# Optimization experiments

Hardware: AMD Instinct MI355X
Metric: run time of the kernel (lower is better)

## Reference

```python
import jax, jax.numpy as jnp
import numpy as np

N_DRUG, N_TARGET, N_EDGES, H = 50000, 20000, 500000, 256


def setup_inputs() -> dict:
    key = jax.random.key(0)
    ks = jax.random.split(key, 6)
    s = 1.0 / np.sqrt(2 * H)
    return {
        "z_drug": jax.random.normal(ks[0], (N_DRUG, H), dtype=jnp.float32),
        "z_target": jax.random.normal(ks[1], (N_TARGET, H), dtype=jnp.float32),
        "row": jax.random.randint(ks[2], (N_EDGES,), 0, N_DRUG, dtype=jnp.int64),
        "col": jax.random.randint(ks[3], (N_EDGES,), 0, N_TARGET, dtype=jnp.int64),
        "W1": jax.random.normal(ks[4], (2 * H, H), dtype=jnp.float32) * s,
        "b1": jnp.zeros((H,), dtype=jnp.float32),
        "W2": jax.random.normal(ks[5], (H, 1), dtype=jnp.float32) * (1.0 / np.sqrt(H)),
        "b2": jnp.zeros((1,), dtype=jnp.float32),
    }


def reference(z_drug, z_target, row, col, W1, b1, W2, b2):
    # gather endpoint embeddings by edge index, concat -> [E, 2H]
    zc = jnp.concatenate([z_drug[row], z_target[col]], axis=-1)
    h = jax.nn.relu(zc @ W1 + b1)          # [E, H]
    return h @ W2 + b2                     # [E, 1]
```

## Files before the change

### kernel.cpp

```cpp
#include <hip/hip_runtime.h>
#include <hip/hip_bf16.h>
#include <stdint.h>


typedef unsigned short u16;
typedef __attribute__((ext_vector_type(8))) short short8;
typedef __attribute__((ext_vector_type(4))) float f32x4;

#define HDIM 256
#define KDIM 512
#define BK 64
#define BIN_SHIFT 4

__device__ __forceinline__ u16 f2bf(float f) {
  union { float f; uint32_t u; } v; v.f = f;
  uint32_t u = v.u;
  return (u16)((u + 0x7fffu + ((u >> 16) & 1u)) >> 16);
}
__device__ __forceinline__ u16 f2h(float f) {
  union { _Float16 h; u16 u; } v; v.h = (_Float16)f;
  return v.u;
}
__device__ __forceinline__ float h2f(u16 b) {
  union { _Float16 h; u16 u; } v; v.u = b;
  return (float)v.h;
}

__device__ __forceinline__ void gl2lds16(const void* g, void* l) {
  __builtin_amdgcn_global_load_lds(
      (const __attribute__((address_space(1))) unsigned int*)g,
      (__attribute__((address_space(3))) unsigned int*)l,
      16, 0, 0);
}

__global__ void prep_w1t(const float* __restrict__ w1, u16* __restrict__ w1t) {
  const int b = blockIdx.x;
  __shared__ float tile[64][65];
  const int k0 = (b >> 2) * 64, n0 = (b & 3) * 64;
  const int tx = threadIdx.x & 63, ty = threadIdx.x >> 6;
#pragma unroll
  for (int i = ty; i < 64; i += 4)
    tile[i][tx] = w1[(size_t)(k0 + i) * HDIM + n0 + tx];
  __syncthreads();
#pragma unroll
  for (int i = ty; i < 64; i += 4)
    w1t[(size_t)(n0 + i) * KDIM + k0 + tx] = f2bf(tile[tx][i]);
}

__global__ void hist_kernel(const int* __restrict__ row, int* __restrict__ bins,
                            int E, int NB) {
  __shared__ int lh[4096];
  for (int i = threadIdx.x; i < NB; i += 256) lh[i] = 0;
  __syncthreads();
  for (int e = blockIdx.x * 256 + threadIdx.x; e < E; e += gridDim.x * 256)
    atomicAdd(&lh[row[e] >> BIN_SHIFT], 1);
  __syncthreads();
  for (int i = threadIdx.x; i < NB; i += 256) {
    int c = lh[i];
    if (c) atomicAdd(&bins[i], c);
  }
}

__global__ void scan_kernel(int* __restrict__ bins, int NB) {
  __shared__ int part[256];
  const int t = threadIdx.x;
  const int per = (NB + 255) / 256;
  const int lo = t * per, hi = min(lo + per, NB);
  int s = 0;
  for (int i = lo; i < hi; ++i) s += bins[i];
  part[t] = s;
  __syncthreads();
  if (t == 0) {
    int a = 0;
    for (int i = 0; i < 256; ++i) { int c = part[i]; part[i] = a; a += c; }
  }
  __syncthreads();
  int run = part[t];
  for (int i = lo; i < hi; ++i) { int c = bins[i]; bins[i] = run; run += c; }
}

__global__ void scatter_kernel(const int* __restrict__ row,
                               int* __restrict__ cursor,
                               int* __restrict__ perm, int E) {
  for (int e = blockIdx.x * 256 + threadIdx.x; e < E; e += gridDim.x * 256) {
    int pos = atomicAdd(&cursor[row[e] >> BIN_SHIFT], 1);
    perm[pos] = e;
  }
}

__global__ __launch_bounds__(256, 2) void uv_gemm(
    const float* __restrict__ zdf, const float* __restrict__ ztf,
    const u16* __restrict__ w1t, const float* __restrict__ b1,
    u16* __restrict__ Uh, u16* __restrict__ Vh,
    int ND, int NT, int nUb) {
  __shared__ u16 lB[2][HDIM * BK];

  const int bid = blockIdx.x;
  const int isV = (bid >= nUb);
  const int lb  = isV ? (bid - nUb) : bid;
  const float* zf = isV ? ztf : zdf;
  u16* Oh = isV ? Vh : Uh;
  const int NR = isV ? NT : ND;
  const int r0 = lb * 128;
  const int kb = isV ? 4 : 0;

  const int tid   = threadIdx.x;
  const int wid   = tid >> 6;
  const int lane  = tid & 63;
  const int r8    = lane >> 3;
  const int slog  = ((lane & 7) ^ (r8 & 7)) * 8;
  const int colid = lane & 15;
  const int quad  = lane >> 4;
  const int csw   = colid & 7;

  const u16* pB = w1t + (uint32_t)(wid * 64 + r8) * KDIM + slog;
  u16* lBw0 = &lB[0][(wid * 64) * BK];
  u16* lBw1 = &lB[1][(wid * 64) * BK];

  uint32_t offR[2];
#pragma unroll
  for (int rt = 0; rt < 2; ++rt) {
    int r = min(r0 + wid * 32 + rt * 16 + colid, NR - 1);
    offR[rt] = (uint32_t)r * HDIM;
  }

  f32x4 acc[2][16];
#pragma unroll
  for (int i = 0; i < 2; ++i)
#pragma unroll
    for (int j = 0; j < 16; ++j) acc[i][j] = f32x4{0.f, 0.f, 0.f, 0.f};

  float4 a32[2][2][2];
  short8 aB[2][2][2];

  auto loadA = [&](int kc) {
#pragma unroll
    for (int rt = 0; rt < 2; ++rt)
#pragma unroll
      for (int s = 0; s < 2; ++s) {
        const float* p = zf + offR[rt] + kc * BK + s * 32 + quad * 8;
        a32[rt][s][0] = ((const float4*)p)[0];
        a32[rt][s][1] = ((const float4*)p)[1];
      }
  };
  auto cvtA = [&](int buf) {
#pragma unroll
    for (int rt = 0; rt < 2; ++rt)
#pragma unroll
      for (int s = 0; s < 2; ++s) {
        float4 lo = a32[rt][s][0], hi = a32[rt][s][1];
        short8 r;
        r[0] = (short)f2bf(lo.x); r[1] = (short)f2bf(lo.y);
        r[2] = (short)f2bf(lo.z); r[3] = (short)f2bf(lo.w);
        r[4] = (short)f2bf(hi.x); r[5] = (short)f2bf(hi.y);
        r[6] = (short)f2bf(hi.z); r[7] = (short)f2bf(hi.w);
        aB[buf][rt][s] = r;
      }
  };
  auto stageB = [&](int kch, u16* dst) {
#pragma unroll
    for (int t = 0; t < 8; ++t)
      gl2lds16(pB + (size_t)t * 8 * KDIM + kch * BK, dst + t * 8 * BK);
  };

  loadA(0);
  stageB(kb, lBw0);
  asm volatile("s_waitcnt vmcnt(0)" ::: "memory");
  cvtA(0);
  __builtin_amdgcn_s_barrier();

#pragma unroll
  for (int kc = 0; kc < 4; ++kc) {
    const int cur = kc & 1, nxt = cur ^ 1;
    if (kc < 3) {
      loadA(kc + 1);
      stageB(kb + kc + 1, nxt ? lBw1 : lBw0);
    }
#pragma unroll
    for (int s = 0; s < 2; ++s) {
      const int sl = s * 4 + quad;
      __builtin_amdgcn_s_setprio(1);
#pragma unroll
      for (int ct = 0; ct < 16; ++ct) {
        short8 bF = *(const short8*)
            &lB[cur][(ct * 16 + colid) * BK + ((sl ^ csw) * 8)];
        acc[0][ct] = __builtin_amdgcn_mfma_f32_16x16x32_bf16(
            aB[cur][0][s], bF, acc[0][ct], 0, 0, 0);
        acc[1][ct] = __builtin_amdgcn_mfma_f32_16x16x32_bf16(
            aB[cur][1][s], bF, acc[1][ct], 0, 0, 0);
      }
      __builtin_amdgcn_s_setprio(0);
    }
    if (kc < 3) {
      asm volatile("s_waitcnt vmcnt(0)" ::: "memory");
      cvtA(nxt);
      __builtin_amdgcn_s_barrier();
    }
  }

  float b1v[16];
#pragma unroll
  for (int ct = 0; ct < 16; ++ct)
    b1v[ct] = isV ? 0.f : b1[ct * 16 + colid];
#pragma unroll
  for (int rt = 0; rt < 2; ++rt)
#pragma unroll
    for (int j = 0; j < 4; ++j) {
      int r = r0 + wid * 32 + rt * 16 + quad * 4 + j;
      if (r < NR) {
#pragma unroll
        for (int ct = 0; ct < 16; ++ct)
          Oh[(size_t)r * HDIM + ct * 16 + colid] =
              f2h(acc[rt][ct][j] + b1v[ct]);
      }
    }
}

__global__ __launch_bounds__(256, 8) void edge_kernel_sorted(
    const u16* __restrict__ U, const u16* __restrict__ V,
    const int* __restrict__ perm,
    const int* __restrict__ row, const int* __restrict__ col,
    const float* __restrict__ w2, const float* __restrict__ b2,
    float* __restrict__ out, int E) {
  const int tid  = threadIdx.x;
  const int lane = tid & 63;
  const int wid  = tid >> 6;
  const int li   = lane & 7;
  const int eg   = lane >> 3;

  float w2v[32];
#pragma unroll
  for (int i = 0; i < 32; ++i) w2v[i] = w2[li * 32 + i];
  const float b2v = b2[0];

  for (int base = blockIdx.x * 32; base < E; base += gridDim.x * 32) {
    const int idx = base + wid * 8 + eg;
    const int ii  = min(idx, E - 1);
    const int pe  = perm[ii];
    const short8* up = (const short8*)(U + (size_t)row[pe] * HDIM + li * 32);
    const short8* vp = (const short8*)(V + (size_t)col[pe] * HDIM + li * 32);
    short8 ub[4], vb[4];
#pragma unroll
    for (int t = 0; t < 4; ++t) { ub[t] = up[t]; vb[t] = vp[t]; }
    float s = 0.f;
#pragma unroll
    for (int t = 0; t < 4; ++t)
#pragma unroll
      for (int i = 0; i < 8; ++i) {
        float h = h2f((u16)ub[t][i]) + h2f((u16)vb[t][i]);
        s += fmaxf(h, 0.f) * w2v[t * 8 + i];
      }
    s += __shfl_xor(s, 1, 8);
    s += __shfl_xor(s, 2, 8);
    s += __shfl_xor(s, 4, 8);
    if (li == 0 && idx < E) out[pe] = s + b2v;
  }
}

__global__ __launch_bounds__(256, 8) void edge_kernel(
    const u16* __restrict__ U, const u16* __restrict__ V,
    const int* __restrict__ row, const int* __restrict__ col,
    const float* __restrict__ w2, const float* __restrict__ b2,
    float* __restrict__ out, int E) {
  const int tid  = threadIdx.x;
  const int lane = tid & 63;
  const int wid  = tid >> 6;
  const int li   = lane & 7;
  const int eg   = lane >> 3;
  float w2v[32];
#pragma unroll
  for (int i = 0; i < 32; ++i) w2v[i] = w2[li * 32 + i];
  const float b2v = b2[0];
  for (int base = blockIdx.x * 32; base < E; base += gridDim.x * 32) {
    const int e  = base + wid * 8 + eg;
    const int ee = min(e, E - 1);
    const short8* up = (const short8*)(U + (size_t)row[ee] * HDIM + li * 32);
    const short8* vp = (const short8*)(V + (size_t)col[ee] * HDIM + li * 32);
    short8 ub[4], vb[4];
#pragma unroll
    for (int t = 0; t < 4; ++t) { ub[t] = up[t]; vb[t] = vp[t]; }
    float s = 0.f;
#pragma unroll
    for (int t = 0; t < 4; ++t)
#pragma unroll
      for (int i = 0; i < 8; ++i) {
        float h = h2f((u16)ub[t][i]) + h2f((u16)vb[t][i]);
        s += fmaxf(h, 0.f) * w2v[t * 8 + i];
      }
    s += __shfl_xor(s, 1, 8);
    s += __shfl_xor(s, 2, 8);
    s += __shfl_xor(s, 4, 8);
    if (li == 0 && e < E) out[e] = s + b2v;
  }
}

__global__ void fallback_kernel(
    const float* __restrict__ zd, const float* __restrict__ zt,
    const int* __restrict__ row, const int* __restrict__ col,
    const float* __restrict__ W1, const float* __restrict__ b1,
    const float* __restrict__ W2, const float* __restrict__ b2,
    float* __restrict__ out, int E) {
  __shared__ float zc[16][512];
  __shared__ float red[4][16];
  const int e0 = blockIdx.x * 16;
  const int tid = threadIdx.x;
  for (int i = tid; i < 16 * 512; i += 256) {
    int e = i >> 9, k = i & 511;
    int ge = min(e0 + e, E - 1);
    zc[e][k] = (k < HDIM) ? zd[(size_t)row[ge] * HDIM + k]
                          : zt[(size_t)col[ge] * HDIM + (k - HDIM)];
  }
  __syncthreads();
  float acc[16];
#pragma unroll
  for (int e = 0; e < 16; ++e) acc[e] = 0.f;
  for (int k = 0; k < KDIM; ++k) {
    float w = W1[k * HDIM + tid];
#pragma unroll
    for (int e = 0; e < 16; ++e) acc[e] += zc[e][k] * w;
  }
  float wv = W2[tid], bv = b1[tid];
  const int lane = tid & 63, wid = tid >> 6;
#pragma unroll
  for (int e = 0; e < 16; ++e) {
    float pv = fmaxf(acc[e] + bv, 0.f) * wv;
#pragma unroll
    for (int off = 32; off >= 1; off >>= 1) pv += __shfl_down(pv, off, 64);
    if (lane == 0) red[wid][e] = pv;
  }
  __syncthreads();
  if (tid < 16) {
    int ge = e0 + tid;
    if (ge < E)
      out[ge] = red[0][tid] + red[1][tid] + red[2][tid] + red[3][tid] + b2[0];
  }
}

extern "C" void kernel_launch(void* const* d_in, const int* in_sizes, int n_in,
                              void* d_out, int out_size, void* d_ws, size_t ws_size,
                              hipStream_t stream) {
  const float* zd_f = (const float*)d_in[0];
  const float* zt_f = (const float*)d_in[1];
  const int*   row  = (const int*)d_in[2];
  const int*   col  = (const int*)d_in[3];
  const float* W1   = (const float*)d_in[4];
  const float* b1   = (const float*)d_in[5];
  const float* W2   = (const float*)d_in[6];
  const float* b2   = (const float*)d_in[7];
  float* out = (float*)d_out;

  const int E  = in_sizes[2];
  const int ND = in_sizes[0] / HDIM;
  const int NT = in_sizes[1] / HDIM;
  const int NB = (ND + (1 << BIN_SHIFT) - 1) >> BIN_SHIFT;

  size_t off_w1t  = 0;
  size_t off_U    = (size_t)KDIM * HDIM * sizeof(u16);
  size_t off_V    = off_U + (size_t)ND * HDIM * sizeof(u16);
  size_t off_bins = off_V + (size_t)NT * HDIM * sizeof(u16);
  size_t off_perm = off_bins + 16384;
  size_t need_sorted = off_perm + (size_t)E * sizeof(int);
  size_t need_plain  = off_bins;

  if (ws_size >= need_plain) {
    u16* w1t = (u16*)((char*)d_ws + off_w1t);
    u16* Uh  = (u16*)((char*)d_ws + off_U);
    u16* Vh  = (u16*)((char*)d_ws + off_V);
    const int nUb = (ND + 127) / 128;
    const int nVb = (NT + 127) / 128;
    prep_w1t<<<32, 256, 0, stream>>>(W1, w1t);
    uv_gemm<<<nUb + nVb, 256, 0, stream>>>(zd_f, zt_f, w1t, b1, Uh, Vh,
                                           ND, NT, nUb);
    int egrid = (E + 31) / 32;
    if (egrid > 2048) egrid = 2048;

    if (ws_size >= need_sorted && NB <= 4096) {
      int* bins = (int*)((char*)d_ws + off_bins);
      int* perm = (int*)((char*)d_ws + off_perm);
      hipMemsetAsync(bins, 0, (size_t)NB * sizeof(int), stream);
      hist_kernel<<<256, 256, 0, stream>>>(row, bins, E, NB);
      scan_kernel<<<1, 256, 0, stream>>>(bins, NB);
      scatter_kernel<<<256, 256, 0, stream>>>(row, bins, perm, E);
      edge_kernel_sorted<<<egrid, 256, 0, stream>>>(Uh, Vh, perm, row, col,
                                                    W2, b2, out, E);
    } else {
      edge_kernel<<<egrid, 256, 0, stream>>>(Uh, Vh, row, col, W2, b2,
                                             out, E);
    }
  } else {
    fallback_kernel<<<(E + 15) / 16, 256, 0, stream>>>(
        zd_f, zt_f, row, col, W1, b1, W2, b2, out, E);
  }
}
```

Measured before the change: 301.3 us.

## Replace fine row sort with 8-bin XCD-aligned edge partition

Drops the histogram, scan and fine-grained scatter pipeline (about 3k bins) for a single scatter pass. That pass splits edges into 8 coarse row-range bins and stores packed (row|col<<16, edge id) int2 entries. The edge kernel maps bin to blockIdx&7, so each block group, which likely lands on one XCD, touches only a slice of U sized to stay in its L2, and it no longer rereads row/col. Within each bin edges are unordered and output writes are scattered. Bins have fixed capacity with no per-bin overflow check, so skewed row distributions could overflow a bin.

```diff
diff --git a/kernel.cpp b/kernel.cpp
--- a/kernel.cpp
+++ b/kernel.cpp
@@ -10,7 +10,7 @@
 #define HDIM 256
 #define KDIM 512
 #define BK 64
-#define BIN_SHIFT 4
+#define BINCAP 66560
 
 __device__ __forceinline__ u16 f2bf(float f) {
   union { float f; uint32_t u; } v; v.f = f;
@@ -47,44 +47,30 @@
     w1t[(size_t)(n0 + i) * KDIM + k0 + tx] = f2bf(tile[tx][i]);
 }
 
-__global__ void hist_kernel(const int* __restrict__ row, int* __restrict__ bins,
-                            int E, int NB) {
-  __shared__ int lh[4096];
-  for (int i = threadIdx.x; i < NB; i += 256) lh[i] = 0;
-  __syncthreads();
-  for (int e = blockIdx.x * 256 + threadIdx.x; e < E; e += gridDim.x * 256)
-    atomicAdd(&lh[row[e] >> BIN_SHIFT], 1);
-  __syncthreads();
-  for (int i = threadIdx.x; i < NB; i += 256) {
-    int c = lh[i];
-    if (c) atomicAdd(&bins[i], c);
-  }
-}
-
-__global__ void scan_kernel(int* __restrict__ bins, int NB) {
-  __shared__ int part[256];
-  const int t = threadIdx.x;
-  const int per = (NB + 255) / 256;
-  const int lo = t * per, hi = min(lo + per, NB);
-  int s = 0;
-  for (int i = lo; i < hi; ++i) s += bins[i];
-  part[t] = s;
-  __syncthreads();
-  if (t == 0) {
-    int a = 0;
-    for (int i = 0; i < 256; ++i) { int c = part[i]; part[i] = a; a += c; }
-  }
-  __syncthreads();
-  int run = part[t];
-  for (int i = lo; i < hi; ++i) { int c = bins[i]; bins[i] = run; run += c; }
-}
-
-__global__ void scatter_kernel(const int* __restrict__ row,
-                               int* __restrict__ cursor,
-                               int* __restrict__ perm, int E) {
-  for (int e = blockIdx.x * 256 + threadIdx.x; e < E; e += gridDim.x * 256) {
-    int pos = atomicAdd(&cursor[row[e] >> BIN_SHIFT], 1);
-    perm[pos] = e;
+__global__ __launch_bounds__(256) void scatter8(
+    const int* __restrict__ row, const int* __restrict__ col,
+    int* __restrict__ cursors, int2* __restrict__ perm,
+    int E, float binScale) {
+  __shared__ int lcnt[8], lbase[8];
+  for (int e0 = blockIdx.x * 256; e0 < E; e0 += gridDim.x * 256) {
+    const int e = e0 + threadIdx.x;
+    const bool v = (e < E);
+    int r = 0, c = 0, bin = 0, rank = 0;
+    if (threadIdx.x < 8) lcnt[threadIdx.x] = 0;
+    __syncthreads();
+    if (v) {
+      r = row[e]; c = col[e];
+      bin = min(7, (int)((float)r * binScale));
+      rank = atomicAdd(&lcnt[bin], 1);
+    }
+    __syncthreads();
+    if (threadIdx.x < 8)
+      lbase[threadIdx.x] = atomicAdd(&cursors[threadIdx.x], lcnt[threadIdx.x]);
+    __syncthreads();
+    if (v) {
+      int pos = lbase[bin] + rank;
+      perm[(size_t)bin * BINCAP + pos] = make_int2(r | (c << 16), e);
+    }
   }
 }
 
@@ -216,29 +202,36 @@
     }
 }
 
-__global__ __launch_bounds__(256, 8) void edge_kernel_sorted(
+__global__ __launch_bounds__(256, 8) void edge_kernel_bins(
     const u16* __restrict__ U, const u16* __restrict__ V,
-    const int* __restrict__ perm,
-    const int* __restrict__ row, const int* __restrict__ col,
+    const int2* __restrict__ perm, const int* __restrict__ cnt,
     const float* __restrict__ w2, const float* __restrict__ b2,
-    float* __restrict__ out, int E) {
+    float* __restrict__ out) {
   const int tid  = threadIdx.x;
   const int lane = tid & 63;
   const int wid  = tid >> 6;
   const int li   = lane & 7;
   const int eg   = lane >> 3;
+  const int bin  = blockIdx.x & 7;
+  const int sub  = blockIdx.x >> 3;
+  const int nsub = gridDim.x >> 3;
 
   float w2v[32];
 #pragma unroll
   for (int i = 0; i < 32; ++i) w2v[i] = w2[li * 32 + i];
   const float b2v = b2[0];
 
-  for (int base = blockIdx.x * 32; base < E; base += gridDim.x * 32) {
+  const int n = cnt[bin];
+  const int2* p = perm + (size_t)bin * BINCAP;
+
+  for (int base = sub * 32; base < n; base += nsub * 32) {
     const int idx = base + wid * 8 + eg;
-    const int ii  = min(idx, E - 1);
-    const int pe  = perm[ii];
-    const short8* up = (const short8*)(U + (size_t)row[pe] * HDIM + li * 32);
-    const short8* vp = (const short8*)(V + (size_t)col[pe] * HDIM + li * 32);
+    const int ii  = min(idx, n - 1);
+    const int2 rc = p[ii];
+    const int r = rc.x & 0xFFFF;
+    const int c = ((unsigned)rc.x) >> 16;
+    const short8* up = (const short8*)(U + (size_t)r * HDIM + li * 32);
+    const short8* vp = (const short8*)(V + (size_t)c * HDIM + li * 32);
     short8 ub[4], vb[4];
 #pragma unroll
     for (int t = 0; t < 4; ++t) { ub[t] = up[t]; vb[t] = vp[t]; }
@@ -253,7 +246,7 @@
     s += __shfl_xor(s, 1, 8);
     s += __shfl_xor(s, 2, 8);
     s += __shfl_xor(s, 4, 8);
-    if (li == 0 && idx < E) out[pe] = s + b2v;
+    if (li == 0 && idx < n) out[rc.y] = s + b2v;
   }
 }
 
@@ -336,6 +329,8 @@
   }
 }
 
+static inline size_t align256(size_t x) { return (x + 255) & ~(size_t)255; }
+
 extern "C" void kernel_launch(void* const* d_in, const int* in_sizes, int n_in,
                               void* d_out, int out_size, void* d_ws, size_t ws_size,
                               hipStream_t stream) {
@@ -352,15 +347,16 @@
   const int E  = in_sizes[2];
   const int ND = in_sizes[0] / HDIM;
   const int NT = in_sizes[1] / HDIM;
-  const int NB = (ND + (1 << BIN_SHIFT) - 1) >> BIN_SHIFT;
-
-  size_t off_w1t  = 0;
-  size_t off_U    = (size_t)KDIM * HDIM * sizeof(u16);
-  size_t off_V    = off_U + (size_t)ND * HDIM * sizeof(u16);
-  size_t off_bins = off_V + (size_t)NT * HDIM * sizeof(u16);
-  size_t off_perm = off_bins + 16384;
-  size_t need_sorted = off_perm + (size_t)E * sizeof(int);
-  size_t need_plain  = off_bins;
+
+  size_t off_w1t = 0;
+  size_t off_U   = align256((size_t)KDIM * HDIM * sizeof(u16));
+  size_t off_V   = align256(off_U + (size_t)ND * HDIM * sizeof(u16));
+  size_t off_cur = align256(off_V + (size_t)NT * HDIM * sizeof(u16));
+  size_t off_pm  = align256(off_cur + 8 * sizeof(int));
+  size_t need_bins  = off_pm + (size_t)8 * BINCAP * sizeof(int2);
+  size_t need_plain = off_cur;
+
+  const bool packOK = (ND <= 65536) && (NT <= 65536) && (E <= 8 * BINCAP);
 
   if (ws_size >= need_plain) {
     u16* w1t = (u16*)((char*)d_ws + off_w1t);
@@ -369,21 +365,22 @@
     const int nUb = (ND + 127) / 128;
     const int nVb = (NT + 127) / 128;
     prep_w1t<<<32, 256, 0, stream>>>(W1, w1t);
-    uv_gemm<<<nUb + nVb, 256, 0, stream>>>(zd_f, zt_f, w1t, b1, Uh, Vh,
-                                           ND, NT, nUb);
-    int egrid = (E + 31) / 32;
-    if (egrid > 2048) egrid = 2048;
-
-    if (ws_size >= need_sorted && NB <= 4096) {
-      int* bins = (int*)((char*)d_ws + off_bins);
-      int* perm = (int*)((char*)d_ws + off_perm);
-      hipMemsetAsync(bins, 0, (size_t)NB * sizeof(int), stream);
-      hist_kernel<<<256, 256, 0, stream>>>(row, bins, E, NB);
-      scan_kernel<<<1, 256, 0, stream>>>(bins, NB);
-      scatter_kernel<<<256, 256, 0, stream>>>(row, bins, perm, E);
-      edge_kernel_sorted<<<egrid, 256, 0, stream>>>(Uh, Vh, perm, row, col,
-                                                    W2, b2, out, E);
+
+    if (ws_size >= need_bins && packOK) {
+      int*  cursors = (int*)((char*)d_ws + off_cur);
+      int2* perm    = (int2*)((char*)d_ws + off_pm);
+      hipMemsetAsync(cursors, 0, 8 * sizeof(int), stream);
+      scatter8<<<512, 256, 0, stream>>>(row, col, cursors, perm, E,
+                                        8.0f / (float)ND);
+      uv_gemm<<<nUb + nVb, 256, 0, stream>>>(zd_f, zt_f, w1t, b1, Uh, Vh,
+                                             ND, NT, nUb);
+      edge_kernel_bins<<<2048, 256, 0, stream>>>(Uh, Vh, perm, cursors,
+                                                 W2, b2, out);
     } else {
+      uv_gemm<<<nUb + nVb, 256, 0, stream>>>(zd_f, zt_f, w1t, b1, Uh, Vh,
+                                             ND, NT, nUb);
+      int egrid = (E + 31) / 32;
+      if (egrid > 2048) egrid = 2048;
       edge_kernel<<<egrid, 256, 0, stream>>>(Uh, Vh, row, col, W2, b2,
                                              out, E);
     }
```

Result: faster. 251.7 us (-16.5%).
